# Performance work log

Measured on AMD Instinct MI355X. Metric: run time of the kernel, lower is better.

Reference implementation:

```python
import jax, jax.numpy as jnp
import numpy as np

NUM_HEADS = 16
THETA = 10000.0
B, S, D = 2, 2048, 1024
D_K = D // NUM_HEADS


def setup_inputs() -> dict:
    key = jax.random.key(0)
    ks = jax.random.split(key, 5)
    s = 0.02
    return {
        "x": jax.random.normal(ks[0], (B, S, D), dtype=jnp.float32),
        "W_q": jax.random.normal(ks[1], (D, D), dtype=jnp.float32) * s,
        "W_k": jax.random.normal(ks[2], (D, D), dtype=jnp.float32) * s,
        "W_v": jax.random.normal(ks[3], (D, D), dtype=jnp.float32) * s,
        "W_o": jax.random.normal(ks[4], (D, D), dtype=jnp.float32) * s,
        "token_positions": jnp.arange(S, dtype=jnp.int32),
    }


def _rope(x, token_positions):
    # x: [..., seq, d_k]; equivalent to the block-diagonal 2x2 rotation matmul
    d2 = x.shape[-1] // 2
    inv_freq = THETA ** (-(2.0 * jnp.arange(d2, dtype=x.dtype)) / x.shape[-1])  # [d2]
    ang = token_positions.astype(x.dtype)[:, None] * inv_freq[None, :]  # [seq, d2]
    cos, sin = jnp.cos(ang), jnp.sin(ang)
    xp = x.reshape(x.shape[:-1] + (d2, 2))
    xe, xo = xp[..., 0], xp[..., 1]
    oe = cos * xe - sin * xo
    oo = sin * xe + cos * xo
    return jnp.stack([oe, oo], axis=-1).reshape(x.shape)


def reference(x, W_q, W_k, W_v, W_o, token_positions):
    seq = x.shape[-2]
    # QKV projections (weights stored as [out, in])
    Q = jnp.einsum('bsd,ed->bse', x, W_q)
    K = jnp.einsum('bsd,ed->bse', x, W_k)
    V = jnp.einsum('bsd,ed->bse', x, W_v)
    def split_heads(t):
        return t.reshape(t.shape[:-1] + (NUM_HEADS, D_K)).swapaxes(-3, -2)  # [b,h,s,dk]
    Q, K, V = split_heads(Q), split_heads(K), split_heads(V)
    Q = _rope(Q, token_positions)
    K = _rope(K, token_positions)
    scale = 1.0 / np.sqrt(D_K)
    scores = jnp.einsum('bhqd,bhkd->bhqk', Q, K) * scale
    causal = jnp.tril(jnp.ones((seq, seq), dtype=bool))
    scores = jnp.where(causal, scores, -jnp.inf)
    probs = jax.nn.softmax(scores, axis=-1)
    out = jnp.einsum('bhqk,bhkd->bhqd', probs, V)
    out = out.swapaxes(-3, -2).reshape(x.shape[:-1] + (D,))
    return jnp.einsum('bse,de->bsd', out, W_o)
```

## Files before the change

### kernel.cpp

```cpp
#include <hip/hip_runtime.h>
#include <hip/hip_bf16.h>
#include <math.h>

#define H_    16
#define DK_   64
#define Dm    1024
#define Bb    2
#define Ss    2048
#define Mrows 4096
#define QSCALE 0.1803368801f

typedef short s16x8 __attribute__((ext_vector_type(8)));
typedef float f32x4 __attribute__((ext_vector_type(4)));
typedef unsigned short u16;
typedef unsigned int u32;

__device__ __forceinline__ u16 f2b(float f) {
  __hip_bfloat16 h = __float2bfloat16(f);
  return *reinterpret_cast<u16*>(&h);
}
__device__ __forceinline__ float b2f(u16 u) {
  __hip_bfloat16 h;
  *reinterpret_cast<u16*>(&h) = u;
  return __bfloat162float(h);
}
__device__ __forceinline__ u32 pkbf(float hi, float lo) {
  return __builtin_amdgcn_perm(__float_as_uint(hi), __float_as_uint(lo), 0x07060302u);
}

#define GLDS(g, l)                                                             \
  __builtin_amdgcn_global_load_lds(                                            \
      (const __attribute__((address_space(1))) unsigned int*)(g),              \
      (__attribute__((address_space(3))) unsigned int*)(l), 16, 0, 0)

__device__ __forceinline__ int SW64(int row, int col) {
  return row * 64 + ((((col >> 3) ^ (row & 7) ^ (row >> 3)) & 7) << 3) + (col & 7);
}

__global__ __launch_bounds__(256) void k_castall(
    const float* __restrict__ x,  const float* __restrict__ Wq,
    const float* __restrict__ Wk, const float* __restrict__ Wv,
    const float* __restrict__ Wo,
    u16* __restrict__ xb,  u16* __restrict__ wqb, u16* __restrict__ wkb,
    u16* __restrict__ wvb, u16* __restrict__ wob,
    const int* __restrict__ pos, float2* __restrict__ tab) {
  if (blockIdx.x >= 8192) {
    int t = (blockIdx.x - 8192) * 256 + threadIdx.x;
    int s = t >> 5, i = t & 31;
    float p = (float)pos[s];
    float ang = p * powf(10000.0f, -(float)i / 32.0f);
    tab[t] = make_float2(cosf(ang), sinf(ang));
    return;
  }
  int i = blockIdx.x * 256 + threadIdx.x;
  const float* s;
  u16* d;
  int off;
  if (i < 1048576) { s = x; d = xb; off = i; }
  else {
    int j = i - 1048576;
    int w = j >> 18;
    off = j & 262143;
    s = (w == 0) ? Wq : (w == 1) ? Wk : (w == 2) ? Wv : Wo;
    d = (w == 0) ? wqb : (w == 1) ? wkb : (w == 2) ? wvb : wob;
  }
  float4 v = reinterpret_cast<const float4*>(s)[off];
  ushort4 o;
  o.x = f2b(v.x); o.y = f2b(v.y); o.z = f2b(v.z); o.w = f2b(v.w);
  reinterpret_cast<ushort4*>(d)[off] = o;
}

__global__ __launch_bounds__(256) void k_ropeK(u16* __restrict__ K,
                                               const float2* __restrict__ tab) {
  int t = blockIdx.x * 256 + threadIdx.x;
  int row = t >> 7;
  int c0 = (t & 127) << 3;
  int i0 = (c0 & 63) >> 1;
  const float2* tb = &tab[(row & (Ss - 1)) * 32 + i0];
  float2 cs[4];
#pragma unroll
  for (int j = 0; j < 4; ++j) cs[j] = tb[j];
  size_t off = (size_t)row * Dm + c0;
  s16x8 k = *reinterpret_cast<const s16x8*>(&K[off]);
  s16x8 ko;
#pragma unroll
  for (int j = 0; j < 4; ++j) {
    float ke = b2f((u16)k[2 * j]), kd = b2f((u16)k[2 * j + 1]);
    ko[2 * j]     = (short)f2b(cs[j].x * ke - cs[j].y * kd);
    ko[2 * j + 1] = (short)f2b(cs[j].y * ke + cs[j].x * kd);
  }
  *reinterpret_cast<s16x8*>(&K[off]) = ko;
}

template <int BN, bool QKV>
__global__ __launch_bounds__(256) void k_gemm(
    const u16* __restrict__ A, const u16* __restrict__ B,
    u16* __restrict__ OQ, u16* __restrict__ OK2, u16* __restrict__ OVT,
    float* __restrict__ OF, int K) {
  constexpr int NFR = BN / 32;
  __shared__ __align__(16) u16 lsA[2][128 * 32];
  __shared__ __align__(16) u16 lsB[2][BN * 32];
  const int tid = threadIdx.x, lane = tid & 63, wave = tid >> 6;
  const int quad = lane >> 4, l16 = lane & 15;
  const int wrow = wave >> 1, wcol = wave & 1;
  const int n0 = blockIdx.x * BN, m0 = blockIdx.y * 128;
  f32x4 acc[4][NFR] = {};

  auto stage = [&](int k0, int bi) {
#pragma unroll
    for (int c = 0; c < 2; ++c) {
      int f = (wave * 2 + c) * 64 + lane;
      int row = f >> 2;
      int gs = (f & 3) ^ ((row >> 1) & 3);
      GLDS(A + (size_t)(m0 + row) * K + k0 + gs * 8, &lsA[bi][(wave * 2 + c) * 512]);
    }
#pragma unroll
    for (int c = 0; c < NFR / 2; ++c) {
      int f = (wave * (NFR / 2) + c) * 64 + lane;
      int row = f >> 2;
      int gs = (f & 3) ^ ((row >> 1) & 3);
      GLDS(B + (size_t)(n0 + row) * K + k0 + gs * 8, &lsB[bi][(wave * (NFR / 2) + c) * 512]);
    }
  };

  stage(0, 0);
  int bi = 0;
  for (int k0 = 0; k0 < K; k0 += 32) {
    __syncthreads();
    if (k0 + 32 < K) stage(k0 + 32, bi ^ 1);
    s16x8 af[4], bfr[NFR];
#pragma unroll
    for (int i = 0; i < 4; ++i) {
      int row = wrow * 64 + i * 16 + l16;
      af[i] = *reinterpret_cast<const s16x8*>(
          &lsA[bi][row * 32 + ((quad ^ ((row >> 1) & 3)) << 3)]);
    }
#pragma unroll
    for (int i = 0; i < NFR; ++i) {
      int row = wcol * (BN / 2) + i * 16 + l16;
      bfr[i] = *reinterpret_cast<const s16x8*>(
          &lsB[bi][row * 32 + ((quad ^ ((row >> 1) & 3)) << 3)]);
    }
#pragma unroll
    for (int mi = 0; mi < 4; ++mi)
#pragma unroll
      for (int ni = 0; ni < NFR; ++ni)
        acc[mi][ni] = __builtin_amdgcn_mfma_f32_16x16x32_bf16(af[mi], bfr[ni], acc[mi][ni], 0, 0, 0);
    bi ^= 1;
  }

  if (QKV) {
    const int which = n0 >> 10;
    const int nbase = (n0 & 1023) + wcol * (BN / 2);
    if (which == 2) {
#pragma unroll
      for (int mi = 0; mi < 4; ++mi)
#pragma unroll
        for (int ni = 0; ni < NFR; ++ni) {
          int row0 = m0 + wrow * 64 + mi * 16 + quad * 4;
          int col  = nbase + ni * 16 + l16;
          int bb = row0 >> 11, s0 = row0 & (Ss - 1);
          ushort4 pk;
          pk.x = f2b(acc[mi][ni][0]); pk.y = f2b(acc[mi][ni][1]);
          pk.z = f2b(acc[mi][ni][2]); pk.w = f2b(acc[mi][ni][3]);
          *reinterpret_cast<ushort4*>(&OVT[((size_t)bb * Dm + col) * Ss + s0]) = pk;
        }
    } else {
      u16* Op = which ? OK2 : OQ;
#pragma unroll
      for (int mi = 0; mi < 4; ++mi)
#pragma unroll
        for (int ni = 0; ni < NFR; ++ni)
#pragma unroll
          for (int r = 0; r < 4; ++r) {
            int row = m0 + wrow * 64 + mi * 16 + quad * 4 + r;
            int col = nbase + ni * 16 + l16;
            Op[(size_t)row * Dm + col] = f2b(acc[mi][ni][r]);
          }
    }
  } else {
#pragma unroll
    for (int mi = 0; mi < 4; ++mi)
#pragma unroll
      for (int ni = 0; ni < NFR; ++ni)
#pragma unroll
        for (int r = 0; r < 4; ++r) {
          int row = m0 + wrow * 64 + mi * 16 + quad * 4 + r;
          int col = n0 + wcol * (BN / 2) + ni * 16 + l16;
          OF[(size_t)row * Dm + col] = acc[mi][ni][r];
        }
  }
}

__global__ __launch_bounds__(256) void k_flash(const u16* __restrict__ Q,
                                               const u16* __restrict__ K,
                                               const u16* __restrict__ VT,
                                               u16* __restrict__ O,
                                               const float2* __restrict__ tab) {
  __shared__ __align__(16) u16 lsK[4][64 * 64];
  __shared__ __align__(16) u16 lsVT[4][64 * 64];
  __shared__ __align__(16) u16 lsP[4][32 * 64];
  const int tid = threadIdx.x, lane = tid & 63, wave = tid >> 6;
  const int quad = lane >> 4, l16 = lane & 15;
  const int bid = blockIdx.x;
  const int bh = bid & 31;
  const int h = bh & (H_ - 1), b = bh >> 4;
  const int g = bid >> 5, a = g & 7, bsel = g >> 3;
  const int qt = bsel ? (15 - a) : a;
  const int q0 = qt * 128;
  const int qbase = q0 + wave * 32;
  const int ktmax_w = (qbase + 31) >> 6;
  const int xorv = (l16 * 2) & 0xE;

  s16x8 qf[2][2];
#pragma unroll
  for (int s = 0; s < 2; ++s) {
    const int qpos = qbase + s * 16 + l16;
    const size_t qoff = (size_t)(b * Ss + qpos) * Dm + h * 64;
    s16x8 r0 = *reinterpret_cast<const s16x8*>(&Q[qoff + quad * 8]);
    s16x8 r1 = *reinterpret_cast<const s16x8*>(&Q[qoff + 32 + quad * 8]);
    const float2* tb = &tab[(qpos & (Ss - 1)) * 32];
#pragma unroll
    for (int kc = 0; kc < 2; ++kc) {
      s16x8 raw = kc ? r1 : r0;
#pragma unroll
      for (int p = 0; p < 4; ++p) {
        float2 cs = tb[kc * 16 + quad * 4 + p];
        float e = b2f((u16)raw[2 * p]), o = b2f((u16)raw[2 * p + 1]);
        qf[s][kc][2 * p]     = (short)f2b((cs.x * e - cs.y * o) * QSCALE);
        qf[s][kc][2 * p + 1] = (short)f2b((cs.y * e + cs.x * o) * QSCALE);
      }
    }
  }
  s16x8 ones;
#pragma unroll
  for (int j = 0; j < 8; ++j) ones[j] = (short)0x3F80;

  f32x4 ot[2][4] = {};
  f32x4 lAcc[2] = {};

  auto stagepair = [&](int pp) {
#pragma unroll
    for (int half = 0; half < 2; ++half) {
      const int kt = pp * 2 + half;
      const int slot = kt & 3;
      const size_t kbase  = (size_t)(b * Ss + kt * 64) * Dm + h * 64;
      const size_t vtbase = ((size_t)b * Dm + h * 64) * Ss + kt * 64;
#pragma unroll
      for (int c = 0; c < 2; ++c) {
        int sl = (wave * 2 + c) * 64 + lane;
        int row = sl >> 3;
        int gg = ((sl & 7) ^ (row & 7) ^ (row >> 3)) & 7;
        GLDS(K  + kbase  + (size_t)row * Dm + gg * 8, &lsK[slot][(wave * 2 + c) * 512]);
        GLDS(VT + vtbase + (size_t)row * Ss + gg * 8, &lsVT[slot][(wave * 2 + c) * 512]);
      }
    }
  };

  stagepair(0);
  for (int pp = 0; pp <= qt; ++pp) {
    __syncthreads();
    if (pp < qt) stagepair(pp + 1);
    const int kt0 = 2 * pp;

    f32x4 st[2][2][4] = {};
#pragma unroll
    for (int half = 0; half < 2; ++half) {
      const int kt = kt0 + half;
      if (kt > ktmax_w) break;
      const int slot = kt & 3;
#pragma unroll
      for (int kc = 0; kc < 2; ++kc)
#pragma unroll
        for (int ni = 0; ni < 4; ++ni) {
          s16x8 kf = *reinterpret_cast<const s16x8*>(
              &lsK[slot][SW64(ni * 16 + l16, kc * 32 + quad * 8)]);
          st[half][0][ni] = __builtin_amdgcn_mfma_f32_16x16x32_bf16(kf, qf[0][kc], st[half][0][ni], 0, 0, 0);
          st[half][1][ni] = __builtin_amdgcn_mfma_f32_16x16x32_bf16(kf, qf[1][kc], st[half][1][ni], 0, 0, 0);
        }
    }
#pragma unroll
    for (int half = 0; half < 2; ++half) {
      const int kt = kt0 + half;
      if (kt > ktmax_w) break;
      const int slot = kt & 3;
      if (kt == ktmax_w) {
#pragma unroll
        for (int s = 0; s < 2; ++s) {
          int gq = qbase + s * 16 + l16;
#pragma unroll
          for (int ni = 0; ni < 4; ++ni)
#pragma unroll
            for (int r = 0; r < 4; ++r)
              if (kt * 64 + ni * 16 + quad * 4 + r > gq) st[half][s][ni][r] = -INFINITY;
        }
      }
#pragma unroll
      for (int s = 0; s < 2; ++s)
#pragma unroll
        for (int ni = 0; ni < 4; ++ni) {
          float e0 = __builtin_amdgcn_exp2f(st[half][s][ni][0]);
          float e1 = __builtin_amdgcn_exp2f(st[half][s][ni][1]);
          float e2 = __builtin_amdgcn_exp2f(st[half][s][ni][2]);
          float e3 = __builtin_amdgcn_exp2f(st[half][s][ni][3]);
          uint2 pk;
          pk.x = pkbf(e1, e0);
          pk.y = pkbf(e3, e2);
          *reinterpret_cast<uint2*>(
              &lsP[wave][(s * 16 + l16) * 64 + (((ni * 4 + quad) ^ xorv) << 2)]) = pk;
        }
#pragma unroll
      for (int kc = 0; kc < 2; ++kc) {
        s16x8 pf0 = *reinterpret_cast<const s16x8*>(
            &lsP[wave][l16 * 64 + (((kc * 8 + quad * 2) ^ xorv) << 2)]);
        s16x8 pf1 = *reinterpret_cast<const s16x8*>(
            &lsP[wave][(16 + l16) * 64 + (((kc * 8 + quad * 2) ^ xorv) << 2)]);
        lAcc[0] = __builtin_amdgcn_mfma_f32_16x16x32_bf16(ones, pf0, lAcc[0], 0, 0, 0);
        lAcc[1] = __builtin_amdgcn_mfma_f32_16x16x32_bf16(ones, pf1, lAcc[1], 0, 0, 0);
#pragma unroll
        for (int ni = 0; ni < 4; ++ni) {
          s16x8 vf = *reinterpret_cast<const s16x8*>(
              &lsVT[slot][SW64(ni * 16 + l16, kc * 32 + quad * 8)]);
          ot[0][ni] = __builtin_amdgcn_mfma_f32_16x16x32_bf16(vf, pf0, ot[0][ni], 0, 0, 0);
          ot[1][ni] = __builtin_amdgcn_mfma_f32_16x16x32_bf16(vf, pf1, ot[1][ni], 0, 0, 0);
        }
      }
    }
  }

#pragma unroll
  for (int s = 0; s < 2; ++s) {
    float inv = 1.0f / lAcc[s][0];
    const size_t obase = (size_t)(b * Ss + qbase + s * 16 + l16) * Dm + h * 64;
#pragma unroll
    for (int ni = 0; ni < 4; ++ni) {
      ushort4 pk;
      pk.x = f2b(ot[s][ni][0] * inv); pk.y = f2b(ot[s][ni][1] * inv);
      pk.z = f2b(ot[s][ni][2] * inv); pk.w = f2b(ot[s][ni][3] * inv);
      *reinterpret_cast<ushort4*>(&O[obase + ni * 16 + quad * 4]) = pk;
    }
  }
}

extern "C" void kernel_launch(void* const* d_in, const int* in_sizes, int n_in,
                              void* d_out, int out_size, void* d_ws, size_t ws_size,
                              hipStream_t stream) {
  const float* x  = (const float*)d_in[0];
  const float* Wq = (const float*)d_in[1];
  const float* Wk = (const float*)d_in[2];
  const float* Wv = (const float*)d_in[3];
  const float* Wo = (const float*)d_in[4];
  const int* pos  = (const int*)d_in[5];
  float* out = (float*)d_out;

  char* w = (char*)d_ws;
  u16* xb  = (u16*)w; w += (size_t)Mrows * Dm * 2;
  u16* wqb = (u16*)w; w += (size_t)Dm * Dm * 2;
  u16* wkb = (u16*)w; w += (size_t)Dm * Dm * 2;
  u16* wvb = (u16*)w; w += (size_t)Dm * Dm * 2;
  u16* wob = (u16*)w; w += (size_t)Dm * Dm * 2;
  u16* Qb  = (u16*)w; w += (size_t)Mrows * Dm * 2;
  u16* Kb  = (u16*)w; w += (size_t)Mrows * Dm * 2;
  u16* VTb = (u16*)w; w += (size_t)Mrows * Dm * 2;
  u16* Ab  = (u16*)w; w += (size_t)Mrows * Dm * 2;
  float2* tabf = (float2*)w; w += (size_t)Ss * 32 * sizeof(float2);

  k_castall<<<8448, 256, 0, stream>>>(x, Wq, Wk, Wv, Wo, xb, wqb, wkb, wvb, wob,
                                      pos, tabf);
  k_gemm<128, true><<<dim3(24, 32), 256, 0, stream>>>(xb, wqb, Qb, Kb, VTb, nullptr, Dm);
  k_ropeK<<<Mrows * Dm / 8 / 256, 256, 0, stream>>>(Kb, tabf);
  k_flash<<<dim3(512), 256, 0, stream>>>(Qb, Kb, VTb, Ab, tabf);
  k_gemm<64, false><<<dim3(16, 32), 256, 0, stream>>>(Ab, wob, nullptr, nullptr, nullptr, out, Dm);
}
```

Measured before the change: 185.5 us.

## Split long causal query tiles across two blocks and combine partials

Long query tiles (qt 8..15) are now split across the KV range into two blocks. Each block writes unnormalized fp32 partial outputs and row sums to a workspace, and a new combine kernel adds the pairs and normalizes. This gives 768 more evenly sized blocks in place of 512 imbalanced ones, and K/V staging changes from paired 4-slot buffering to per-tile double buffering. In exchange it adds an extra launch and fp32 partial traffic to global memory. Merging without a running max relies on the existing no-max softmax.

```diff
diff --git a/kernel.cpp b/kernel.cpp
--- a/kernel.cpp
+++ b/kernel.cpp
@@ -196,19 +196,22 @@
                                                const u16* __restrict__ K,
                                                const u16* __restrict__ VT,
                                                u16* __restrict__ O,
+                                               float* __restrict__ Pp_all,
+                                               float* __restrict__ Lp_all,
                                                const float2* __restrict__ tab) {
-  __shared__ __align__(16) u16 lsK[4][64 * 64];
-  __shared__ __align__(16) u16 lsVT[4][64 * 64];
+  __shared__ __align__(16) u16 lsK[2][64 * 64];
+  __shared__ __align__(16) u16 lsVT[2][64 * 64];
   __shared__ __align__(16) u16 lsP[4][32 * 64];
   const int tid = threadIdx.x, lane = tid & 63, wave = tid >> 6;
   const int quad = lane >> 4, l16 = lane & 15;
   const int bid = blockIdx.x;
-  const int bh = bid & 31;
+  const int bh = bid & 31, item = bid >> 5;
   const int h = bh & (H_ - 1), b = bh >> 4;
-  const int g = bid >> 5, a = g & 7, bsel = g >> 3;
-  const int qt = bsel ? (15 - a) : a;
-  const int q0 = qt * 128;
-  const int qbase = q0 + wave * 32;
+  const int j = item & 7, grp = item >> 3;
+  const int qt = (grp == 0) ? j : (15 - j);
+  const int kt_lo = (grp == 2) ? (qt + 1) : 0;
+  const int kt_hi = (grp == 1) ? (qt + 1) : (2 * qt + 2);
+  const int qbase = qt * 128 + wave * 32;
   const int ktmax_w = (qbase + 31) >> 6;
   const int xorv = (l16 * 2) & 0xE;
 
@@ -234,111 +237,135 @@
   }
   s16x8 ones;
 #pragma unroll
-  for (int j = 0; j < 8; ++j) ones[j] = (short)0x3F80;
+  for (int jj = 0; jj < 8; ++jj) ones[jj] = (short)0x3F80;
 
   f32x4 ot[2][4] = {};
   f32x4 lAcc[2] = {};
 
-  auto stagepair = [&](int pp) {
-#pragma unroll
-    for (int half = 0; half < 2; ++half) {
-      const int kt = pp * 2 + half;
-      const int slot = kt & 3;
-      const size_t kbase  = (size_t)(b * Ss + kt * 64) * Dm + h * 64;
-      const size_t vtbase = ((size_t)b * Dm + h * 64) * Ss + kt * 64;
-#pragma unroll
-      for (int c = 0; c < 2; ++c) {
-        int sl = (wave * 2 + c) * 64 + lane;
-        int row = sl >> 3;
-        int gg = ((sl & 7) ^ (row & 7) ^ (row >> 3)) & 7;
-        GLDS(K  + kbase  + (size_t)row * Dm + gg * 8, &lsK[slot][(wave * 2 + c) * 512]);
-        GLDS(VT + vtbase + (size_t)row * Ss + gg * 8, &lsVT[slot][(wave * 2 + c) * 512]);
-      }
+  auto stage = [&](int kt, int bi) {
+    const size_t kbase  = (size_t)(b * Ss + kt * 64) * Dm + h * 64;
+    const size_t vtbase = ((size_t)b * Dm + h * 64) * Ss + kt * 64;
+#pragma unroll
+    for (int c = 0; c < 2; ++c) {
+      int sl = (wave * 2 + c) * 64 + lane;
+      int row = sl >> 3;
+      int gg = ((sl & 7) ^ (row & 7) ^ (row >> 3)) & 7;
+      GLDS(K  + kbase  + (size_t)row * Dm + gg * 8, &lsK[bi][(wave * 2 + c) * 512]);
+      GLDS(VT + vtbase + (size_t)row * Ss + gg * 8, &lsVT[bi][(wave * 2 + c) * 512]);
     }
   };
 
-  stagepair(0);
-  for (int pp = 0; pp <= qt; ++pp) {
+  stage(kt_lo, 0);
+  int bi = 0;
+  for (int kt = kt_lo; kt < kt_hi; ++kt) {
     __syncthreads();
-    if (pp < qt) stagepair(pp + 1);
-    const int kt0 = 2 * pp;
-
-    f32x4 st[2][2][4] = {};
-#pragma unroll
-    for (int half = 0; half < 2; ++half) {
-      const int kt = kt0 + half;
-      if (kt > ktmax_w) break;
-      const int slot = kt & 3;
-#pragma unroll
-      for (int kc = 0; kc < 2; ++kc)
-#pragma unroll
-        for (int ni = 0; ni < 4; ++ni) {
-          s16x8 kf = *reinterpret_cast<const s16x8*>(
-              &lsK[slot][SW64(ni * 16 + l16, kc * 32 + quad * 8)]);
-          st[half][0][ni] = __builtin_amdgcn_mfma_f32_16x16x32_bf16(kf, qf[0][kc], st[half][0][ni], 0, 0, 0);
-          st[half][1][ni] = __builtin_amdgcn_mfma_f32_16x16x32_bf16(kf, qf[1][kc], st[half][1][ni], 0, 0, 0);
-        }
-    }
-#pragma unroll
-    for (int half = 0; half < 2; ++half) {
-      const int kt = kt0 + half;
-      if (kt > ktmax_w) break;
-      const int slot = kt & 3;
-      if (kt == ktmax_w) {
-#pragma unroll
-        for (int s = 0; s < 2; ++s) {
-          int gq = qbase + s * 16 + l16;
-#pragma unroll
-          for (int ni = 0; ni < 4; ++ni)
-#pragma unroll
-            for (int r = 0; r < 4; ++r)
-              if (kt * 64 + ni * 16 + quad * 4 + r > gq) st[half][s][ni][r] = -INFINITY;
-        }
-      }
-#pragma unroll
-      for (int s = 0; s < 2; ++s)
-#pragma unroll
-        for (int ni = 0; ni < 4; ++ni) {
-          float e0 = __builtin_amdgcn_exp2f(st[half][s][ni][0]);
-          float e1 = __builtin_amdgcn_exp2f(st[half][s][ni][1]);
-          float e2 = __builtin_amdgcn_exp2f(st[half][s][ni][2]);
-          float e3 = __builtin_amdgcn_exp2f(st[half][s][ni][3]);
-          uint2 pk;
-          pk.x = pkbf(e1, e0);
-          pk.y = pkbf(e3, e2);
-          *reinterpret_cast<uint2*>(
-              &lsP[wave][(s * 16 + l16) * 64 + (((ni * 4 + quad) ^ xorv) << 2)]) = pk;
-        }
-#pragma unroll
-      for (int kc = 0; kc < 2; ++kc) {
-        s16x8 pf0 = *reinterpret_cast<const s16x8*>(
-            &lsP[wave][l16 * 64 + (((kc * 8 + quad * 2) ^ xorv) << 2)]);
-        s16x8 pf1 = *reinterpret_cast<const s16x8*>(
-            &lsP[wave][(16 + l16) * 64 + (((kc * 8 + quad * 2) ^ xorv) << 2)]);
-        lAcc[0] = __builtin_amdgcn_mfma_f32_16x16x32_bf16(ones, pf0, lAcc[0], 0, 0, 0);
-        lAcc[1] = __builtin_amdgcn_mfma_f32_16x16x32_bf16(ones, pf1, lAcc[1], 0, 0, 0);
-#pragma unroll
-        for (int ni = 0; ni < 4; ++ni) {
-          s16x8 vf = *reinterpret_cast<const s16x8*>(
-              &lsVT[slot][SW64(ni * 16 + l16, kc * 32 + quad * 8)]);
-          ot[0][ni] = __builtin_amdgcn_mfma_f32_16x16x32_bf16(vf, pf0, ot[0][ni], 0, 0, 0);
-          ot[1][ni] = __builtin_amdgcn_mfma_f32_16x16x32_bf16(vf, pf1, ot[1][ni], 0, 0, 0);
-        }
-      }
-    }
-  }
-
-#pragma unroll
-  for (int s = 0; s < 2; ++s) {
-    float inv = 1.0f / lAcc[s][0];
-    const size_t obase = (size_t)(b * Ss + qbase + s * 16 + l16) * Dm + h * 64;
-#pragma unroll
-    for (int ni = 0; ni < 4; ++ni) {
-      ushort4 pk;
-      pk.x = f2b(ot[s][ni][0] * inv); pk.y = f2b(ot[s][ni][1] * inv);
-      pk.z = f2b(ot[s][ni][2] * inv); pk.w = f2b(ot[s][ni][3] * inv);
-      *reinterpret_cast<ushort4*>(&O[obase + ni * 16 + quad * 4]) = pk;
-    }
+    if (kt + 1 < kt_hi) stage(kt + 1, bi ^ 1);
+    if (kt > ktmax_w) { bi ^= 1; continue; }
+
+    f32x4 st[2][4] = {};
+#pragma unroll
+    for (int kc = 0; kc < 2; ++kc)
+#pragma unroll
+      for (int ni = 0; ni < 4; ++ni) {
+        s16x8 kf = *reinterpret_cast<const s16x8*>(
+            &lsK[bi][SW64(ni * 16 + l16, kc * 32 + quad * 8)]);
+        st[0][ni] = __builtin_amdgcn_mfma_f32_16x16x32_bf16(kf, qf[0][kc], st[0][ni], 0, 0, 0);
+        st[1][ni] = __builtin_amdgcn_mfma_f32_16x16x32_bf16(kf, qf[1][kc], st[1][ni], 0, 0, 0);
+      }
+    if (kt == ktmax_w) {
+#pragma unroll
+      for (int s = 0; s < 2; ++s) {
+        int gq = qbase + s * 16 + l16;
+#pragma unroll
+        for (int ni = 0; ni < 4; ++ni)
+#pragma unroll
+          for (int r = 0; r < 4; ++r)
+            if (kt * 64 + ni * 16 + quad * 4 + r > gq) st[s][ni][r] = -INFINITY;
+      }
+    }
+#pragma unroll
+    for (int s = 0; s < 2; ++s)
+#pragma unroll
+      for (int ni = 0; ni < 4; ++ni) {
+        float e0 = __builtin_amdgcn_exp2f(st[s][ni][0]);
+        float e1 = __builtin_amdgcn_exp2f(st[s][ni][1]);
+        float e2 = __builtin_amdgcn_exp2f(st[s][ni][2]);
+        float e3 = __builtin_amdgcn_exp2f(st[s][ni][3]);
+        uint2 pk;
+        pk.x = pkbf(e1, e0);
+        pk.y = pkbf(e3, e2);
+        *reinterpret_cast<uint2*>(
+            &lsP[wave][(s * 16 + l16) * 64 + (((ni * 4 + quad) ^ xorv) << 2)]) = pk;
+      }
+#pragma unroll
+    for (int kc = 0; kc < 2; ++kc) {
+      s16x8 pf0 = *reinterpret_cast<const s16x8*>(
+          &lsP[wave][l16 * 64 + (((kc * 8 + quad * 2) ^ xorv) << 2)]);
+      s16x8 pf1 = *reinterpret_cast<const s16x8*>(
+          &lsP[wave][(16 + l16) * 64 + (((kc * 8 + quad * 2) ^ xorv) << 2)]);
+      lAcc[0] = __builtin_amdgcn_mfma_f32_16x16x32_bf16(ones, pf0, lAcc[0], 0, 0, 0);
+      lAcc[1] = __builtin_amdgcn_mfma_f32_16x16x32_bf16(ones, pf1, lAcc[1], 0, 0, 0);
+#pragma unroll
+      for (int ni = 0; ni < 4; ++ni) {
+        s16x8 vf = *reinterpret_cast<const s16x8*>(
+            &lsVT[bi][SW64(ni * 16 + l16, kc * 32 + quad * 8)]);
+        ot[0][ni] = __builtin_amdgcn_mfma_f32_16x16x32_bf16(vf, pf0, ot[0][ni], 0, 0, 0);
+        ot[1][ni] = __builtin_amdgcn_mfma_f32_16x16x32_bf16(vf, pf1, ot[1][ni], 0, 0, 0);
+      }
+    }
+    bi ^= 1;
+  }
+
+  if (grp == 0) {
+#pragma unroll
+    for (int s = 0; s < 2; ++s) {
+      float inv = 1.0f / lAcc[s][0];
+      const size_t obase = (size_t)(b * Ss + qbase + s * 16 + l16) * Dm + h * 64;
+#pragma unroll
+      for (int ni = 0; ni < 4; ++ni) {
+        ushort4 pk;
+        pk.x = f2b(ot[s][ni][0] * inv); pk.y = f2b(ot[s][ni][1] * inv);
+        pk.z = f2b(ot[s][ni][2] * inv); pk.w = f2b(ot[s][ni][3] * inv);
+        *reinterpret_cast<ushort4*>(&O[obase + ni * 16 + quad * 4]) = pk;
+      }
+    }
+  } else {
+    const int unit = (grp - 1) * 256 + bh * 8 + j;
+    float* Pp = Pp_all + (size_t)unit * 8192;
+    float* Lp = Lp_all + unit * 128;
+#pragma unroll
+    for (int s = 0; s < 2; ++s) {
+      int qlocal = wave * 32 + s * 16 + l16;
+#pragma unroll
+      for (int ni = 0; ni < 4; ++ni)
+        *reinterpret_cast<f32x4*>(&Pp[qlocal * 64 + ni * 16 + quad * 4]) = ot[s][ni];
+      if (quad == 0) Lp[qlocal] = lAcc[s][0];
+    }
+  }
+}
+
+__global__ __launch_bounds__(256) void k_combine(const float* __restrict__ Pp_all,
+                                                 const float* __restrict__ Lp_all,
+                                                 u16* __restrict__ O) {
+  const int u = blockIdx.x;
+  const int bh = u >> 3, j = u & 7, qt = 15 - j;
+  const int h = bh & (H_ - 1), b = bh >> 4;
+  const float* pa = Pp_all + (size_t)u * 8192;
+  const float* pb = pa + (size_t)256 * 8192;
+  const float* la = Lp_all + u * 128;
+  const float* lb = la + 256 * 128;
+#pragma unroll
+  for (int it = 0; it < 8; ++it) {
+    int idx = it * 1024 + threadIdx.x * 4;
+    int q = idx >> 6, dk = idx & 63;
+    float4 va = *reinterpret_cast<const float4*>(pa + idx);
+    float4 vb = *reinterpret_cast<const float4*>(pb + idx);
+    float inv = 1.0f / (la[q] + lb[q]);
+    ushort4 pk;
+    pk.x = f2b((va.x + vb.x) * inv); pk.y = f2b((va.y + vb.y) * inv);
+    pk.z = f2b((va.z + vb.z) * inv); pk.w = f2b((va.w + vb.w) * inv);
+    int gq = qt * 128 + q;
+    *reinterpret_cast<ushort4*>(&O[(size_t)(b * Ss + gq) * Dm + h * 64 + dk]) = pk;
   }
 }
 
@@ -364,11 +391,14 @@
   u16* VTb = (u16*)w; w += (size_t)Mrows * Dm * 2;
   u16* Ab  = (u16*)w; w += (size_t)Mrows * Dm * 2;
   float2* tabf = (float2*)w; w += (size_t)Ss * 32 * sizeof(float2);
+  float* Pp = (float*)w; w += (size_t)512 * 8192 * 4;
+  float* Lp = (float*)w; w += (size_t)512 * 128 * 4;
 
   k_castall<<<8448, 256, 0, stream>>>(x, Wq, Wk, Wv, Wo, xb, wqb, wkb, wvb, wob,
                                       pos, tabf);
   k_gemm<128, true><<<dim3(24, 32), 256, 0, stream>>>(xb, wqb, Qb, Kb, VTb, nullptr, Dm);
   k_ropeK<<<Mrows * Dm / 8 / 256, 256, 0, stream>>>(Kb, tabf);
-  k_flash<<<dim3(512), 256, 0, stream>>>(Qb, Kb, VTb, Ab, tabf);
+  k_flash<<<dim3(768), 256, 0, stream>>>(Qb, Kb, VTb, Ab, Pp, Lp, tabf);
+  k_combine<<<dim3(256), 256, 0, stream>>>(Pp, Lp, Ab);
   k_gemm<64, false><<<dim3(16, 32), 256, 0, stream>>>(Ab, wob, nullptr, nullptr, nullptr, out, Dm);
 }
```

Result: no change. 189.1 us (+1.9%).

## Split output-projection GEMM K dimension across two wave teams per block

Applied to the files above, without the earlier changes.

The Wo projection GEMM now runs 512-thread blocks in which two teams of four waves each handle half of the K=1024 reduction over separate LDS buffers. Their partial accumulators are then summed through shared memory before the fp32 store. The goal is more waves per output tile and half the serial K loop, which helps latency hiding on a grid of only 512 blocks. In exchange it uses more LDS and adds an extra reduction step with syncs. The QKV GEMM is de-templated with no change in behaviour.

```diff
diff --git a/kernel.cpp b/kernel.cpp
--- a/kernel.cpp
+++ b/kernel.cpp
@@ -92,18 +92,17 @@
   *reinterpret_cast<s16x8*>(&K[off]) = ko;
 }
 
-template <int BN, bool QKV>
-__global__ __launch_bounds__(256) void k_gemm(
+__global__ __launch_bounds__(256) void k_gemm_qkv(
     const u16* __restrict__ A, const u16* __restrict__ B,
-    u16* __restrict__ OQ, u16* __restrict__ OK2, u16* __restrict__ OVT,
-    float* __restrict__ OF, int K) {
-  constexpr int NFR = BN / 32;
+    u16* __restrict__ OQ, u16* __restrict__ OK2, u16* __restrict__ OVT) {
+  constexpr int BN = 128, NFR = 4;
   __shared__ __align__(16) u16 lsA[2][128 * 32];
   __shared__ __align__(16) u16 lsB[2][BN * 32];
   const int tid = threadIdx.x, lane = tid & 63, wave = tid >> 6;
   const int quad = lane >> 4, l16 = lane & 15;
   const int wrow = wave >> 1, wcol = wave & 1;
   const int n0 = blockIdx.x * BN, m0 = blockIdx.y * 128;
+  const int K = Dm;
   f32x4 acc[4][NFR] = {};
 
   auto stage = [&](int k0, int bi) {
@@ -115,11 +114,11 @@
       GLDS(A + (size_t)(m0 + row) * K + k0 + gs * 8, &lsA[bi][(wave * 2 + c) * 512]);
     }
 #pragma unroll
-    for (int c = 0; c < NFR / 2; ++c) {
-      int f = (wave * (NFR / 2) + c) * 64 + lane;
+    for (int c = 0; c < 2; ++c) {
+      int f = (wave * 2 + c) * 64 + lane;
       int row = f >> 2;
       int gs = (f & 3) ^ ((row >> 1) & 3);
-      GLDS(B + (size_t)(n0 + row) * K + k0 + gs * 8, &lsB[bi][(wave * (NFR / 2) + c) * 512]);
+      GLDS(B + (size_t)(n0 + row) * K + k0 + gs * 8, &lsB[bi][(wave * 2 + c) * 512]);
     }
   };
 
@@ -137,7 +136,7 @@
     }
 #pragma unroll
     for (int i = 0; i < NFR; ++i) {
-      int row = wcol * (BN / 2) + i * 16 + l16;
+      int row = wcol * 64 + i * 16 + l16;
       bfr[i] = *reinterpret_cast<const s16x8*>(
           &lsB[bi][row * 32 + ((quad ^ ((row >> 1) & 3)) << 3)]);
     }
@@ -149,36 +148,23 @@
     bi ^= 1;
   }
 
-  if (QKV) {
-    const int which = n0 >> 10;
-    const int nbase = (n0 & 1023) + wcol * (BN / 2);
-    if (which == 2) {
-#pragma unroll
-      for (int mi = 0; mi < 4; ++mi)
-#pragma unroll
-        for (int ni = 0; ni < NFR; ++ni) {
-          int row0 = m0 + wrow * 64 + mi * 16 + quad * 4;
-          int col  = nbase + ni * 16 + l16;
-          int bb = row0 >> 11, s0 = row0 & (Ss - 1);
-          ushort4 pk;
-          pk.x = f2b(acc[mi][ni][0]); pk.y = f2b(acc[mi][ni][1]);
-          pk.z = f2b(acc[mi][ni][2]); pk.w = f2b(acc[mi][ni][3]);
-          *reinterpret_cast<ushort4*>(&OVT[((size_t)bb * Dm + col) * Ss + s0]) = pk;
-        }
-    } else {
-      u16* Op = which ? OK2 : OQ;
-#pragma unroll
-      for (int mi = 0; mi < 4; ++mi)
-#pragma unroll
-        for (int ni = 0; ni < NFR; ++ni)
-#pragma unroll
-          for (int r = 0; r < 4; ++r) {
-            int row = m0 + wrow * 64 + mi * 16 + quad * 4 + r;
-            int col = nbase + ni * 16 + l16;
-            Op[(size_t)row * Dm + col] = f2b(acc[mi][ni][r]);
-          }
-    }
+  const int which = n0 >> 10;
+  const int nbase = (n0 & 1023) + wcol * 64;
+  if (which == 2) {
+#pragma unroll
+    for (int mi = 0; mi < 4; ++mi)
+#pragma unroll
+      for (int ni = 0; ni < NFR; ++ni) {
+        int row0 = m0 + wrow * 64 + mi * 16 + quad * 4;
+        int col  = nbase + ni * 16 + l16;
+        int bb = row0 >> 11, s0 = row0 & (Ss - 1);
+        ushort4 pk;
+        pk.x = f2b(acc[mi][ni][0]); pk.y = f2b(acc[mi][ni][1]);
+        pk.z = f2b(acc[mi][ni][2]); pk.w = f2b(acc[mi][ni][3]);
+        *reinterpret_cast<ushort4*>(&OVT[((size_t)bb * Dm + col) * Ss + s0]) = pk;
+      }
   } else {
+    u16* Op = which ? OK2 : OQ;
 #pragma unroll
     for (int mi = 0; mi < 4; ++mi)
 #pragma unroll
@@ -186,9 +172,94 @@
 #pragma unroll
         for (int r = 0; r < 4; ++r) {
           int row = m0 + wrow * 64 + mi * 16 + quad * 4 + r;
-          int col = n0 + wcol * (BN / 2) + ni * 16 + l16;
-          OF[(size_t)row * Dm + col] = acc[mi][ni][r];
-        }
+          int col = nbase + ni * 16 + l16;
+          Op[(size_t)row * Dm + col] = f2b(acc[mi][ni][r]);
+        }
+  }
+}
+
+__global__ __launch_bounds__(512) void k_wo(
+    const u16* __restrict__ A, const u16* __restrict__ B,
+    float* __restrict__ OF) {
+  __shared__ __align__(16) u16 lsA[2][2][128 * 32];
+  __shared__ __align__(16) u16 lsB[2][2][64 * 32];
+  const int tid = threadIdx.x, lane = tid & 63, wave = tid >> 6;
+  const int team = wave >> 2, wv = wave & 3;
+  const int quad = lane >> 4, l16 = lane & 15;
+  const int wrow = wv >> 1, wcol = wv & 1;
+  const int n0 = blockIdx.x * 64, m0 = blockIdx.y * 128;
+  const int kbase = team * 512;
+  f32x4 acc[4][2] = {};
+
+  auto stage = [&](int k0, int bi) {
+#pragma unroll
+    for (int c = 0; c < 2; ++c) {
+      int f = (wv * 2 + c) * 64 + lane;
+      int row = f >> 2;
+      int gs = (f & 3) ^ ((row >> 1) & 3);
+      GLDS(A + (size_t)(m0 + row) * Dm + kbase + k0 + gs * 8,
+           &lsA[team][bi][(wv * 2 + c) * 512]);
+    }
+    {
+      int f = wv * 64 + lane;
+      int row = f >> 2;
+      int gs = (f & 3) ^ ((row >> 1) & 3);
+      GLDS(B + (size_t)(n0 + row) * Dm + kbase + k0 + gs * 8,
+           &lsB[team][bi][wv * 512]);
+    }
+  };
+
+  stage(0, 0);
+  int bi = 0;
+  for (int k0 = 0; k0 < 512; k0 += 32) {
+    __syncthreads();
+    if (k0 + 32 < 512) stage(k0 + 32, bi ^ 1);
+    s16x8 af[4], bfr[2];
+#pragma unroll
+    for (int i = 0; i < 4; ++i) {
+      int row = wrow * 64 + i * 16 + l16;
+      af[i] = *reinterpret_cast<const s16x8*>(
+          &lsA[team][bi][row * 32 + ((quad ^ ((row >> 1) & 3)) << 3)]);
+    }
+#pragma unroll
+    for (int i = 0; i < 2; ++i) {
+      int row = wcol * 32 + i * 16 + l16;
+      bfr[i] = *reinterpret_cast<const s16x8*>(
+          &lsB[team][bi][row * 32 + ((quad ^ ((row >> 1) & 3)) << 3)]);
+    }
+#pragma unroll
+    for (int mi = 0; mi < 4; ++mi)
+#pragma unroll
+      for (int ni = 0; ni < 2; ++ni)
+        acc[mi][ni] = __builtin_amdgcn_mfma_f32_16x16x32_bf16(af[mi], bfr[ni], acc[mi][ni], 0, 0, 0);
+    bi ^= 1;
+  }
+
+  __syncthreads();
+  float* scr = (float*)&lsA[0][0][0];
+  const int ttid = tid & 255;
+  if (team == 1) {
+#pragma unroll
+    for (int mi = 0; mi < 4; ++mi)
+#pragma unroll
+      for (int ni = 0; ni < 2; ++ni)
+        *reinterpret_cast<f32x4*>(&scr[(mi * 2 + ni) * 1024 + ttid * 4]) = acc[mi][ni];
+  }
+  __syncthreads();
+  if (team == 0) {
+#pragma unroll
+    for (int mi = 0; mi < 4; ++mi)
+#pragma unroll
+      for (int ni = 0; ni < 2; ++ni) {
+        f32x4 other = *reinterpret_cast<const f32x4*>(&scr[(mi * 2 + ni) * 1024 + ttid * 4]);
+        f32x4 v = acc[mi][ni] + other;
+#pragma unroll
+        for (int r = 0; r < 4; ++r) {
+          int row = m0 + wrow * 64 + mi * 16 + quad * 4 + r;
+          int col = n0 + wcol * 32 + ni * 16 + l16;
+          OF[(size_t)row * Dm + col] = v[r];
+        }
+      }
   }
 }
 
@@ -367,8 +438,8 @@
 
   k_castall<<<8448, 256, 0, stream>>>(x, Wq, Wk, Wv, Wo, xb, wqb, wkb, wvb, wob,
                                       pos, tabf);
-  k_gemm<128, true><<<dim3(24, 32), 256, 0, stream>>>(xb, wqb, Qb, Kb, VTb, nullptr, Dm);
+  k_gemm_qkv<<<dim3(24, 32), 256, 0, stream>>>(xb, wqb, Qb, Kb, VTb);
   k_ropeK<<<Mrows * Dm / 8 / 256, 256, 0, stream>>>(Kb, tabf);
   k_flash<<<dim3(512), 256, 0, stream>>>(Qb, Kb, VTb, Ab, tabf);
-  k_gemm<64, false><<<dim3(16, 32), 256, 0, stream>>>(Ab, wob, nullptr, nullptr, nullptr, out, Dm);
-}
+  k_wo<<<dim3(16, 32), 512, 0, stream>>>(Ab, wob, out);
+}
```

Measured after the change: 186.6 us. About the same (+0.6%).
